# Kernel optimization log

Measured on AMD Instinct MI355X. Metric: run time of the kernel, lower is better.

The kernel has to match this reference:

```python
import jax, jax.numpy as jnp
import numpy as np

NEG_INF = -1e30


def setup_inputs() -> dict:
    key = jax.random.key(0)
    k1, k2 = jax.random.split(key)
    B, S, H, D = 2, 2048, 16, 64
    qkv = jax.random.normal(k1, (B, S, 3, H, D), dtype=jnp.float32)
    pos_bias = jax.random.normal(k2, (H, S, S), dtype=jnp.float32)
    return {"qkv": qkv, "pos_bias": pos_bias}


def reference(qkv, pos_bias):
    # qkv: (B, S, 3, H, D); fixed-length path of FlashAttention.forward
    # (key_padding_mask=None, cu_seqlens=None) -> standard per-batch attention
    # with additive per-head positional bias and causal masking.
    B, S, _, H, D = qkv.shape
    q = qkv[:, :, 0]  # (B, S, H, D)
    k = qkv[:, :, 1]
    v = qkv[:, :, 2]
    softmax_scale = 1.0 / jnp.sqrt(jnp.asarray(D, dtype=qkv.dtype))
    # scores: (B, H, S, S)
    scores = jnp.einsum('bshd,bthd->bhst', q, k) * softmax_scale
    scores = scores + pos_bias[None]  # broadcast bias over batch
    # causal mask (query s attends to keys t <= s)
    causal = jnp.tril(jnp.ones((S, S), dtype=bool))
    scores = jnp.where(causal[None, None], scores, NEG_INF)
    attn = jax.nn.softmax(scores, axis=-1)
    # output: (B, S, H, D)
    out = jnp.einsum('bhst,bthd->bshd', attn, v)
    return out
```

## Files before the change

kernel.cpp:

```cpp
#include <hip/hip_runtime.h>

typedef float f32x4 __attribute__((ext_vector_type(4)));
typedef __bf16 bf16x8 __attribute__((ext_vector_type(8)));

#define MFMA16(a, b, c) __builtin_amdgcn_mfma_f32_16x16x32_bf16(a, b, c, 0, 0, 0)

constexpr int Bn = 2, S = 2048, H = 16, Dh = 64;
constexpr int BR = 64, BC = 64;
constexpr int KSTR = Dh + 8;
constexpr int VSTR = BC + 8;
constexpr int PSTR = BC + 8;
#define NEG_INF_F (-1e30f)

__global__ __launch_bounds__(256, 4) void fa_fwd(
    const float* __restrict__ qkv,
    const float* __restrict__ pb,
    float* __restrict__ out)
{
    __shared__ __bf16 klds[BC][KSTR];
    __shared__ __bf16 vlds[Dh][VSTR];
    __shared__ __bf16 plds[4][16][PSTR];

    const int tid  = threadIdx.x;
    const int wave = tid >> 6;
    const int lane = tid & 63;
    const int quad = lane >> 4;
    const int l16  = lane & 15;

    const int bid = blockIdx.x;
    const int g   = bid >> 8;
    const int pp  = bid & 255;
    const int kk  = pp >> 5;
    const int hb  = pp & 31;
    const int b   = hb & 1;
    const int h   = hb >> 1;
    const int qt  = (g == 0) ? 31 - kk : (g == 1) ? 16 + kk : (g == 2) ? 15 - kk : kk;
    const int q0  = qt * BR;

    const float scale = 0.125f;

    const int qrow = q0 + wave * 16 + l16;
    const float* qp = qkv + (((size_t)(b * S + qrow) * 3 + 0) * H + h) * Dh;
    bf16x8 qfrag[2];
#pragma unroll
    for (int ks = 0; ks < 2; ++ks) {
        f32x4 a = *(const f32x4*)(qp + ks * 32 + quad * 8);
        f32x4 c = *(const f32x4*)(qp + ks * 32 + quad * 8 + 4);
#pragma unroll
        for (int j = 0; j < 4; ++j) qfrag[ks][j] = (__bf16)a[j];
#pragma unroll
        for (int j = 0; j < 4; ++j) qfrag[ks][4 + j] = (__bf16)c[j];
    }

    const int myrow = q0 + wave * 16 + quad * 4;
    float l_r[4] = {0.f, 0.f, 0.f, 0.f};
    f32x4 oacc[4];
#pragma unroll
    for (int dt = 0; dt < 4; ++dt) oacc[dt] = (f32x4){0.f, 0.f, 0.f, 0.f};

    const int srow = tid >> 2;
    const int scol = (tid & 3) * 16;
    const int vd   = tid & 63;
    const int vt0  = (tid >> 6) * 16;
    constexpr int VT_STRIDE = 3 * H * Dh;

    const float* kbase = qkv + (((size_t)(b * S + srow) * 3 + 1) * H + h) * Dh + scol;
    const float* vbase = qkv + (((size_t)(b * S + vt0) * 3 + 2) * H + h) * Dh + vd;
    const float* bbase = pb + (size_t)h * S * S + (size_t)myrow * S + l16;

    float kreg[16], vreg[16], breg[16];

    {
        *(f32x4*)&kreg[0]  = *(const f32x4*)(kbase + 0);
        *(f32x4*)&kreg[4]  = *(const f32x4*)(kbase + 4);
        *(f32x4*)&kreg[8]  = *(const f32x4*)(kbase + 8);
        *(f32x4*)&kreg[12] = *(const f32x4*)(kbase + 12);
#pragma unroll
        for (int i = 0; i < 16; ++i) vreg[i] = vbase[(size_t)i * VT_STRIDE];
#pragma unroll
        for (int ct = 0; ct < 4; ++ct)
#pragma unroll
            for (int r = 0; r < 4; ++r) breg[ct * 4 + r] = bbase[(size_t)r * S + ct * 16];
    }

    const int niter = qt + 1;
    for (int it = 0; it < niter; ++it) {
        __syncthreads();

        {
            bf16x8 t0, t1;
#pragma unroll
            for (int i = 0; i < 8; ++i) { t0[i] = (__bf16)kreg[i]; t1[i] = (__bf16)kreg[8 + i]; }
            *(bf16x8*)&klds[srow][scol]     = t0;
            *(bf16x8*)&klds[srow][scol + 8] = t1;
#pragma unroll
            for (int i = 0; i < 8; ++i) { t0[i] = (__bf16)vreg[i]; t1[i] = (__bf16)vreg[8 + i]; }
            *(bf16x8*)&vlds[vd][vt0]     = t0;
            *(bf16x8*)&vlds[vd][vt0 + 8] = t1;
        }

        float bcur[16];
#pragma unroll
        for (int i = 0; i < 16; ++i) bcur[i] = breg[i];

        if (it + 1 < niter) {
            const size_t joff = (size_t)(it + 1) * BC;
            const float* kp = kbase + joff * VT_STRIDE;
            const float* vp = vbase + joff * VT_STRIDE;
            const float* bp = bbase + joff;
            *(f32x4*)&kreg[0]  = *(const f32x4*)(kp + 0);
            *(f32x4*)&kreg[4]  = *(const f32x4*)(kp + 4);
            *(f32x4*)&kreg[8]  = *(const f32x4*)(kp + 8);
            *(f32x4*)&kreg[12] = *(const f32x4*)(kp + 12);
#pragma unroll
            for (int i = 0; i < 16; ++i) vreg[i] = vp[(size_t)i * VT_STRIDE];
#pragma unroll
            for (int ct = 0; ct < 4; ++ct)
#pragma unroll
                for (int r = 0; r < 4; ++r) breg[ct * 4 + r] = bp[(size_t)r * S + ct * 16];
        }

        __syncthreads();

        f32x4 sacc[4];
#pragma unroll
        for (int ct = 0; ct < 4; ++ct) sacc[ct] = (f32x4){0.f, 0.f, 0.f, 0.f};
#pragma unroll
        for (int ct = 0; ct < 4; ++ct) {
#pragma unroll
            for (int ks = 0; ks < 2; ++ks) {
                bf16x8 kf = *(const bf16x8*)&klds[ct * 16 + l16][ks * 32 + quad * 8];
                sacc[ct] = MFMA16(qfrag[ks], kf, sacc[ct]);
            }
        }

        const bool diag = (it == niter - 1);
#pragma unroll
        for (int ct = 0; ct < 4; ++ct) {
            const int colrel = ct * 16 + l16;
#pragma unroll
            for (int r = 0; r < 4; ++r) {
                float s = fmaf(sacc[ct][r], scale, bcur[ct * 4 + r]);
                if (diag && (q0 + colrel > myrow + r)) s = NEG_INF_F;
                float p = __expf(s);
                l_r[r] += p;
                plds[wave][quad * 4 + r][colrel] = (__bf16)p;
            }
        }

        bf16x8 pf[2];
#pragma unroll
        for (int ks = 0; ks < 2; ++ks)
            pf[ks] = *(const bf16x8*)&plds[wave][l16][ks * 32 + quad * 8];
#pragma unroll
        for (int dt = 0; dt < 4; ++dt) {
#pragma unroll
            for (int ks = 0; ks < 2; ++ks) {
                bf16x8 vf = *(const bf16x8*)&vlds[dt * 16 + l16][ks * 32 + quad * 8];
                oacc[dt] = MFMA16(pf[ks], vf, oacc[dt]);
            }
        }
    }

#pragma unroll
    for (int r = 0; r < 4; ++r) {
#pragma unroll
        for (int m = 1; m < 16; m <<= 1) l_r[r] += __shfl_xor(l_r[r], m, 64);
        const float inv = 1.0f / l_r[r];
        float* op = out + (((size_t)(b * S + (myrow + r)) * H) + h) * Dh;
#pragma unroll
        for (int dt = 0; dt < 4; ++dt)
            op[dt * 16 + l16] = oacc[dt][r] * inv;
    }
}

extern "C" void kernel_launch(void* const* d_in, const int* in_sizes, int n_in,
                              void* d_out, int out_size, void* d_ws, size_t ws_size,
                              hipStream_t stream) {
    const float* qkv = (const float*)d_in[0];
    const float* pb  = (const float*)d_in[1];
    float* out       = (float*)d_out;
    fa_fwd<<<dim3(Bn * H * (S / BR)), dim3(256), 0, stream>>>(qkv, pb, out);
}
```

Measured before the change: 424.3 us.

## Split causal KV loop across two blocks by tile parity and add combine kernel

Each query tile's key/value iterations are divided between two blocks, one taking even tiles and one taking odd tiles. Each block writes an unnormalized partial output and row sum to workspace, and a separate combine kernel adds the two partials and normalizes. This doubles the grid to 2048 blocks for better load balance and occupancy, and the launch-bounds hint moves from 4 to 5 blocks per CU. The cost is an extra kernel launch plus workspace traffic for the partials. The kernel uses no running max, so the partial sums can be added directly without rescaling.

```diff
diff --git a/kernel.cpp b/kernel.cpp
--- a/kernel.cpp
+++ b/kernel.cpp
@@ -12,10 +12,14 @@
 constexpr int PSTR = BC + 8;
 #define NEG_INF_F (-1e30f)
 
-__global__ __launch_bounds__(256, 4) void fa_fwd(
+template<bool SPLIT>
+__global__ __launch_bounds__(256, 5) void fa_fwd(
     const float* __restrict__ qkv,
     const float* __restrict__ pb,
-    float* __restrict__ out)
+    float* __restrict__ po0,
+    float* __restrict__ po1,
+    float* __restrict__ pl0,
+    float* __restrict__ pl1)
 {
     __shared__ __bf16 klds[BC][KSTR];
     __shared__ __bf16 vlds[Dh][VSTR];
@@ -27,15 +31,28 @@
     const int quad = lane >> 4;
     const int l16  = lane & 15;
 
-    const int bid = blockIdx.x;
-    const int g   = bid >> 8;
-    const int pp  = bid & 255;
-    const int kk  = pp >> 5;
-    const int hb  = pp & 31;
-    const int b   = hb & 1;
-    const int h   = hb >> 1;
-    const int qt  = (g == 0) ? 31 - kk : (g == 1) ? 16 + kk : (g == 2) ? 15 - kk : kk;
-    const int q0  = qt * BR;
+    int b, h, qt, parity;
+    if (SPLIT) {
+        const int u  = blockIdx.x >> 8;
+        const int v  = blockIdx.x & 255;
+        const int bh = v >> 3;
+        const int s  = v & 7;
+        b = bh & 1; h = bh >> 1;
+        const int j = s * 8 + ((s & 1) ? 7 - u : u);
+        qt = 31 - (j >> 1);
+        parity = j & 1;
+    } else {
+        const int g  = blockIdx.x >> 8;
+        const int pp = blockIdx.x & 255;
+        const int kk = pp >> 5;
+        const int hb = pp & 31;
+        b = hb & 1; h = hb >> 1;
+        qt = (g == 0) ? 31 - kk : (g == 1) ? 16 + kk : (g == 2) ? 15 - kk : kk;
+        parity = 0;
+    }
+    const int q0   = qt * BR;
+    const int STEP = SPLIT ? 2 : 1;
+    const int it0  = SPLIT ? parity : 0;
 
     const float scale = 0.125f;
 
@@ -71,20 +88,23 @@
     float kreg[16], vreg[16], breg[16];
 
     {
-        *(f32x4*)&kreg[0]  = *(const f32x4*)(kbase + 0);
-        *(f32x4*)&kreg[4]  = *(const f32x4*)(kbase + 4);
-        *(f32x4*)&kreg[8]  = *(const f32x4*)(kbase + 8);
-        *(f32x4*)&kreg[12] = *(const f32x4*)(kbase + 12);
-#pragma unroll
-        for (int i = 0; i < 16; ++i) vreg[i] = vbase[(size_t)i * VT_STRIDE];
+        const size_t j0 = (size_t)it0 * BC;
+        const float* kp = kbase + j0 * VT_STRIDE;
+        const float* vp = vbase + j0 * VT_STRIDE;
+        const float* bp = bbase + j0;
+        *(f32x4*)&kreg[0]  = *(const f32x4*)(kp + 0);
+        *(f32x4*)&kreg[4]  = *(const f32x4*)(kp + 4);
+        *(f32x4*)&kreg[8]  = *(const f32x4*)(kp + 8);
+        *(f32x4*)&kreg[12] = *(const f32x4*)(kp + 12);
+#pragma unroll
+        for (int i = 0; i < 16; ++i) vreg[i] = vp[(size_t)i * VT_STRIDE];
 #pragma unroll
         for (int ct = 0; ct < 4; ++ct)
 #pragma unroll
-            for (int r = 0; r < 4; ++r) breg[ct * 4 + r] = bbase[(size_t)r * S + ct * 16];
-    }
-
-    const int niter = qt + 1;
-    for (int it = 0; it < niter; ++it) {
+            for (int r = 0; r < 4; ++r) breg[ct * 4 + r] = bp[(size_t)r * S + ct * 16];
+    }
+
+    for (int it = it0; it <= qt; it += STEP) {
         __syncthreads();
 
         {
@@ -103,8 +123,8 @@
 #pragma unroll
         for (int i = 0; i < 16; ++i) bcur[i] = breg[i];
 
-        if (it + 1 < niter) {
-            const size_t joff = (size_t)(it + 1) * BC;
+        if (it + STEP <= qt) {
+            const size_t joff = (size_t)(it + STEP) * BC;
             const float* kp = kbase + joff * VT_STRIDE;
             const float* vp = vbase + joff * VT_STRIDE;
             const float* bp = bbase + joff;
@@ -134,14 +154,14 @@
             }
         }
 
-        const bool diag = (it == niter - 1);
+        const bool diag = (it == qt);
 #pragma unroll
         for (int ct = 0; ct < 4; ++ct) {
             const int colrel = ct * 16 + l16;
 #pragma unroll
             for (int r = 0; r < 4; ++r) {
                 float s = fmaf(sacc[ct][r], scale, bcur[ct * 4 + r]);
-                if (diag && (q0 + colrel > myrow + r)) s = NEG_INF_F;
+                if (diag && (colrel > wave * 16 + quad * 4 + r)) s = NEG_INF_F;
                 float p = __expf(s);
                 l_r[r] += p;
                 plds[wave][quad * 4 + r][colrel] = (__bf16)p;
@@ -162,16 +182,40 @@
         }
     }
 
+    float* po = (SPLIT && parity) ? po1 : po0;
+    float* pl = (SPLIT && parity) ? pl1 : pl0;
 #pragma unroll
     for (int r = 0; r < 4; ++r) {
 #pragma unroll
         for (int m = 1; m < 16; m <<= 1) l_r[r] += __shfl_xor(l_r[r], m, 64);
-        const float inv = 1.0f / l_r[r];
-        float* op = out + (((size_t)(b * S + (myrow + r)) * H) + h) * Dh;
-#pragma unroll
-        for (int dt = 0; dt < 4; ++dt)
-            op[dt * 16 + l16] = oacc[dt][r] * inv;
-    }
+        const int row = myrow + r;
+        float* op = po + (((size_t)(b * S + row) * H) + h) * Dh;
+        if (SPLIT) {
+#pragma unroll
+            for (int dt = 0; dt < 4; ++dt)
+                op[dt * 16 + l16] = oacc[dt][r];
+            if (l16 == 0) pl[(size_t)(b * S + row) * H + h] = l_r[r];
+        } else {
+            const float inv = 1.0f / l_r[r];
+#pragma unroll
+            for (int dt = 0; dt < 4; ++dt)
+                op[dt * 16 + l16] = oacc[dt][r] * inv;
+        }
+    }
+}
+
+__global__ __launch_bounds__(256, 8) void fa_combine(
+    const float* __restrict__ po0, const float* __restrict__ po1,
+    const float* __restrict__ pl0, const float* __restrict__ pl1,
+    float* __restrict__ out)
+{
+    const size_t f4  = (size_t)blockIdx.x * 256 + threadIdx.x;
+    const size_t idx = f4 * 4;
+    const size_t rr  = idx >> 6;
+    const float inv = 1.0f / (pl0[rr] + pl1[rr]);
+    f32x4 a = *(const f32x4*)(po0 + idx);
+    f32x4 c = *(const f32x4*)(po1 + idx);
+    *(f32x4*)(out + idx) = (a + c) * inv;
 }
 
 extern "C" void kernel_launch(void* const* d_in, const int* in_sizes, int n_in,
@@ -180,5 +224,19 @@
     const float* qkv = (const float*)d_in[0];
     const float* pb  = (const float*)d_in[1];
     float* out       = (float*)d_out;
-    fa_fwd<<<dim3(Bn * H * (S / BR)), dim3(256), 0, stream>>>(qkv, pb, out);
+
+    constexpr size_t PO_ELEMS = (size_t)Bn * S * H * Dh;
+    constexpr size_t PL_ELEMS = (size_t)Bn * S * H;
+    constexpr size_t WS_NEEDED = (2 * PO_ELEMS + 2 * PL_ELEMS) * sizeof(float);
+
+    if (ws_size >= WS_NEEDED) {
+        float* po0 = (float*)d_ws;
+        float* po1 = po0 + PO_ELEMS;
+        float* pl0 = po1 + PO_ELEMS;
+        float* pl1 = pl0 + PL_ELEMS;
+        fa_fwd<true><<<dim3(2048), dim3(256), 0, stream>>>(qkv, pb, po0, po1, pl0, pl1);
+        fa_combine<<<dim3((unsigned)(PO_ELEMS / 4 / 256)), dim3(256), 0, stream>>>(po0, po1, pl0, pl1, out);
+    } else {
+        fa_fwd<false><<<dim3(1024), dim3(256), 0, stream>>>(qkv, pb, out, nullptr, nullptr, nullptr);
+    }
 }
```

Measured after the change: 814.0 us. 1.92x slower.

## Precompute bf16 swizzled K and transposed V, load via global_load_lds

Applied to the files above, without the earlier changes.

Adds a prep kernel that converts K to bf16 with an XOR-swizzled layout and writes V transposed in bf16 into the workspace. The attention kernel then copies these tiles straight into LDS with global_load_lds, replacing per-iteration fp32 loads, conversions and strided V gathers, and its LDS reads use the swizzle instead of padding. The register prefetch double-buffering of K/V/bias is dropped, so the bias loads now sit on the critical path each iteration, and the extra launch adds a pass over K and V.

```diff
diff --git a/kernel.cpp b/kernel.cpp
--- a/kernel.cpp
+++ b/kernel.cpp
@@ -5,21 +5,73 @@
 
 #define MFMA16(a, b, c) __builtin_amdgcn_mfma_f32_16x16x32_bf16(a, b, c, 0, 0, 0)
 
-constexpr int Bn = 2, S = 2048, H = 16, Dh = 64;
+constexpr int S = 2048, H = 16, Dh = 64;
 constexpr int BR = 64, BC = 64;
-constexpr int KSTR = Dh + 8;
-constexpr int VSTR = BC + 8;
-constexpr int PSTR = BC + 8;
 #define NEG_INF_F (-1e30f)
 
+__device__ __forceinline__ void gld16(const __bf16* g, __bf16* l) {
+    __builtin_amdgcn_global_load_lds(
+        (const __attribute__((address_space(1))) void*)(g),
+        (__attribute__((address_space(3))) void*)(l), 16, 0, 0);
+}
+
+__global__ __launch_bounds__(256) void prep(const float* __restrict__ qkv,
+                                            __bf16* __restrict__ khat,
+                                            __bf16* __restrict__ vT)
+{
+    __shared__ __bf16 vtile[64][72];
+    const int tid = threadIdx.x;
+    const int bid = blockIdx.x;
+    const int tt  = bid & 31;
+    const int bh  = bid >> 5;
+    const int b   = bh >> 4, h = bh & 15;
+    const int t0  = tt * 64;
+    const int tr  = tid >> 2, c0 = (tid & 3) * 16;
+
+    const float* kp = qkv + (((size_t)(b * S + t0 + tr) * 3 + 1) * H + h) * Dh + c0;
+    const float* vp = qkv + (((size_t)(b * S + t0 + tr) * 3 + 2) * H + h) * Dh + c0;
+    f32x4 k0 = *(const f32x4*)(kp + 0), k1 = *(const f32x4*)(kp + 4),
+          k2 = *(const f32x4*)(kp + 8), k3 = *(const f32x4*)(kp + 12);
+    f32x4 v0 = *(const f32x4*)(vp + 0), v1 = *(const f32x4*)(vp + 4),
+          v2 = *(const f32x4*)(vp + 8), v3 = *(const f32x4*)(vp + 12);
+    bf16x8 ka, kb, va, vb;
+#pragma unroll
+    for (int j = 0; j < 4; ++j) {
+        ka[j] = (__bf16)k0[j]; ka[4 + j] = (__bf16)k1[j];
+        kb[j] = (__bf16)k2[j]; kb[4 + j] = (__bf16)k3[j];
+        va[j] = (__bf16)v0[j]; va[4 + j] = (__bf16)v1[j];
+        vb[j] = (__bf16)v2[j]; vb[4 + j] = (__bf16)v3[j];
+    }
+    {
+        __bf16* kd = khat + ((size_t)bh * S + t0 + tr) * Dh;
+        const int g0 = c0 >> 3, sw = tr & 7;
+        *(bf16x8*)(kd + ((( g0    ) ^ sw) << 3)) = ka;
+        *(bf16x8*)(kd + (((g0 + 1) ^ sw) << 3)) = kb;
+    }
+    *(bf16x8*)&vtile[tr][c0]     = va;
+    *(bf16x8*)&vtile[tr][c0 + 8] = vb;
+    __syncthreads();
+    const int d = tid >> 2, tc0 = (tid & 3) * 16;
+    bf16x8 x, y;
+#pragma unroll
+    for (int i = 0; i < 8; ++i) {
+        x[i] = vtile[tc0 + i][d];
+        y[i] = vtile[tc0 + 8 + i][d];
+    }
+    __bf16* vd = vT + ((size_t)bh * Dh + d) * S + t0;
+    const int h0 = tc0 >> 3, sv = d & 7;
+    *(bf16x8*)(vd + ((( h0    ) ^ sv) << 3)) = x;
+    *(bf16x8*)(vd + (((h0 + 1) ^ sv) << 3)) = y;
+}
+
 __global__ __launch_bounds__(256, 4) void fa_fwd(
-    const float* __restrict__ qkv,
-    const float* __restrict__ pb,
+    const float* __restrict__ qkv, const float* __restrict__ pb,
+    const __bf16* __restrict__ khat, const __bf16* __restrict__ vT,
     float* __restrict__ out)
 {
-    __shared__ __bf16 klds[BC][KSTR];
-    __shared__ __bf16 vlds[Dh][VSTR];
-    __shared__ __bf16 plds[4][16][PSTR];
+    __shared__ __bf16 klds[64 * 64];
+    __shared__ __bf16 vlds[64 * 64];
+    __shared__ __bf16 plds[4][16][72];
 
     const int tid  = threadIdx.x;
     const int wave = tid >> 6;
@@ -27,16 +79,13 @@
     const int quad = lane >> 4;
     const int l16  = lane & 15;
 
-    const int bid = blockIdx.x;
-    const int g   = bid >> 8;
-    const int pp  = bid & 255;
-    const int kk  = pp >> 5;
-    const int hb  = pp & 31;
-    const int b   = hb & 1;
-    const int h   = hb >> 1;
-    const int qt  = (g == 0) ? 31 - kk : (g == 1) ? 16 + kk : (g == 2) ? 15 - kk : kk;
-    const int q0  = qt * BR;
-
+    const int g  = blockIdx.x >> 8;
+    const int pp = blockIdx.x & 255;
+    const int kk = pp >> 5, hb = pp & 31;
+    const int b  = hb & 1, h = hb >> 1;
+    const int qt = (g == 0) ? 31 - kk : (g == 1) ? 16 + kk : (g == 2) ? 15 - kk : kk;
+    const int q0 = qt * BR;
+    const int bh = b * H + h;
     const float scale = 0.125f;
 
     const int qrow = q0 + wave * 16 + l16;
@@ -52,76 +101,39 @@
         for (int j = 0; j < 4; ++j) qfrag[ks][4 + j] = (__bf16)c[j];
     }
 
-    const int myrow = q0 + wave * 16 + quad * 4;
+    const int lrow  = wave * 16 + quad * 4;
+    const int myrow = q0 + lrow;
     float l_r[4] = {0.f, 0.f, 0.f, 0.f};
     f32x4 oacc[4];
 #pragma unroll
     for (int dt = 0; dt < 4; ++dt) oacc[dt] = (f32x4){0.f, 0.f, 0.f, 0.f};
 
-    const int srow = tid >> 2;
-    const int scol = (tid & 3) * 16;
-    const int vd   = tid & 63;
-    const int vt0  = (tid >> 6) * 16;
-    constexpr int VT_STRIDE = 3 * H * Dh;
-
-    const float* kbase = qkv + (((size_t)(b * S + srow) * 3 + 1) * H + h) * Dh + scol;
-    const float* vbase = qkv + (((size_t)(b * S + vt0) * 3 + 2) * H + h) * Dh + vd;
-    const float* bbase = pb + (size_t)h * S * S + (size_t)myrow * S + l16;
-
-    float kreg[16], vreg[16], breg[16];
-
-    {
-        *(f32x4*)&kreg[0]  = *(const f32x4*)(kbase + 0);
-        *(f32x4*)&kreg[4]  = *(const f32x4*)(kbase + 4);
-        *(f32x4*)&kreg[8]  = *(const f32x4*)(kbase + 8);
-        *(f32x4*)&kreg[12] = *(const f32x4*)(kbase + 12);
-#pragma unroll
-        for (int i = 0; i < 16; ++i) vreg[i] = vbase[(size_t)i * VT_STRIDE];
+    const int seg = wave * 2;
+    const int lt  = lane >> 3, le = (lane & 7) * 8;
+    const __bf16* kg = khat + ((size_t)bh * S + (seg * 8 + lt)) * 64 + le;
+    const __bf16* vg = vT   + ((size_t)bh * Dh + seg * 8 + lt) * S + le;
+    __bf16* kl = klds + seg * 512;
+    __bf16* vl = vlds + seg * 512;
+
+    const float* bb = pb + (size_t)h * S * S + (size_t)myrow * S + l16;
+    const int swz = l16 & 7;
+
+    for (int it = 0; it <= qt; ++it) {
+        __syncthreads();
+        gld16(kg,         kl);
+        gld16(kg + 512,   kl + 512);
+        gld16(vg,         vl);
+        gld16(vg + 8 * S, vl + 512);
+        kg += BC * 64; vg += BC;
+
+        float breg[16];
 #pragma unroll
         for (int ct = 0; ct < 4; ++ct)
 #pragma unroll
-            for (int r = 0; r < 4; ++r) breg[ct * 4 + r] = bbase[(size_t)r * S + ct * 16];
-    }
-
-    const int niter = qt + 1;
-    for (int it = 0; it < niter; ++it) {
+            for (int r = 0; r < 4; ++r) breg[ct * 4 + r] = bb[(size_t)r * S + ct * 16];
+        bb += BC;
         __syncthreads();
 
-        {
-            bf16x8 t0, t1;
-#pragma unroll
-            for (int i = 0; i < 8; ++i) { t0[i] = (__bf16)kreg[i]; t1[i] = (__bf16)kreg[8 + i]; }
-            *(bf16x8*)&klds[srow][scol]     = t0;
-            *(bf16x8*)&klds[srow][scol + 8] = t1;
-#pragma unroll
-            for (int i = 0; i < 8; ++i) { t0[i] = (__bf16)vreg[i]; t1[i] = (__bf16)vreg[8 + i]; }
-            *(bf16x8*)&vlds[vd][vt0]     = t0;
-            *(bf16x8*)&vlds[vd][vt0 + 8] = t1;
-        }
-
-        float bcur[16];
-#pragma unroll
-        for (int i = 0; i < 16; ++i) bcur[i] = breg[i];
-
-        if (it + 1 < niter) {
-            const size_t joff = (size_t)(it + 1) * BC;
-            const float* kp = kbase + joff * VT_STRIDE;
-            const float* vp = vbase + joff * VT_STRIDE;
-            const float* bp = bbase + joff;
-            *(f32x4*)&kreg[0]  = *(const f32x4*)(kp + 0);
-            *(f32x4*)&kreg[4]  = *(const f32x4*)(kp + 4);
-            *(f32x4*)&kreg[8]  = *(const f32x4*)(kp + 8);
-            *(f32x4*)&kreg[12] = *(const f32x4*)(kp + 12);
-#pragma unroll
-            for (int i = 0; i < 16; ++i) vreg[i] = vp[(size_t)i * VT_STRIDE];
-#pragma unroll
-            for (int ct = 0; ct < 4; ++ct)
-#pragma unroll
-                for (int r = 0; r < 4; ++r) breg[ct * 4 + r] = bp[(size_t)r * S + ct * 16];
-        }
-
-        __syncthreads();
-
         f32x4 sacc[4];
 #pragma unroll
         for (int ct = 0; ct < 4; ++ct) sacc[ct] = (f32x4){0.f, 0.f, 0.f, 0.f};
@@ -129,19 +141,19 @@
         for (int ct = 0; ct < 4; ++ct) {
 #pragma unroll
             for (int ks = 0; ks < 2; ++ks) {
-                bf16x8 kf = *(const bf16x8*)&klds[ct * 16 + l16][ks * 32 + quad * 8];
+                bf16x8 kf = *(const bf16x8*)&klds[(ct * 16 + l16) * 64 + (((ks * 4 + quad) ^ swz) << 3)];
                 sacc[ct] = MFMA16(qfrag[ks], kf, sacc[ct]);
             }
         }
 
-        const bool diag = (it == niter - 1);
+        const bool diag = (it == qt);
 #pragma unroll
         for (int ct = 0; ct < 4; ++ct) {
             const int colrel = ct * 16 + l16;
 #pragma unroll
             for (int r = 0; r < 4; ++r) {
-                float s = fmaf(sacc[ct][r], scale, bcur[ct * 4 + r]);
-                if (diag && (q0 + colrel > myrow + r)) s = NEG_INF_F;
+                float s = fmaf(sacc[ct][r], scale, breg[ct * 4 + r]);
+                if (diag && (colrel > lrow + r)) s = NEG_INF_F;
                 float p = __expf(s);
                 l_r[r] += p;
                 plds[wave][quad * 4 + r][colrel] = (__bf16)p;
@@ -156,7 +168,7 @@
         for (int dt = 0; dt < 4; ++dt) {
 #pragma unroll
             for (int ks = 0; ks < 2; ++ks) {
-                bf16x8 vf = *(const bf16x8*)&vlds[dt * 16 + l16][ks * 32 + quad * 8];
+                bf16x8 vf = *(const bf16x8*)&vlds[(dt * 16 + l16) * 64 + (((ks * 4 + quad) ^ swz) << 3)];
                 oacc[dt] = MFMA16(pf[ks], vf, oacc[dt]);
             }
         }
@@ -180,5 +192,11 @@
     const float* qkv = (const float*)d_in[0];
     const float* pb  = (const float*)d_in[1];
     float* out       = (float*)d_out;
-    fa_fwd<<<dim3(Bn * H * (S / BR)), dim3(256), 0, stream>>>(qkv, pb, out);
-}
+
+    constexpr size_t KV_ELEMS = (size_t)2 * H * S * Dh;
+    __bf16* khat = (__bf16*)d_ws;
+    __bf16* vT   = khat + KV_ELEMS;
+
+    prep<<<dim3(1024), dim3(256), 0, stream>>>(qkv, khat, vT);
+    fa_fwd<<<dim3(1024), dim3(256), 0, stream>>>(qkv, pb, khat, vT, out);
+}
```

New measurement: 404.7 us. 1.05x faster.
